# Optimization experiments

Measured on AMD Instinct MI355X. Metric: run time of the kernel, lower is better.

## Reference

```python
import jax, jax.numpy as jnp
import numpy as np

B, N, C = 16, 65536, 21          # batch, anchors, classes (class 0 = background)
TH_CONF = 0.05                   # confidence threshold
TH_IOU = 0.5                     # NMS IoU threshold
TOP_K = 200                      # candidates kept per (batch, class) before NMS
V0, V1 = 0.1, 0.2                # SSD box-coder variances


def setup_inputs() -> dict:
    key = jax.random.key(0)
    k1, k2, k3, k4 = jax.random.split(key, 4)
    conf = jax.random.normal(k1, (B, N, C), dtype=jnp.float32)
    loc = jax.random.normal(k2, (B, N, 4), dtype=jnp.float32)
    # anchors in center form (cx, cy, w, h), normalized coords
    cxcy = jax.random.uniform(k3, (N, 2), dtype=jnp.float32)
    wh = 0.02 + 0.2 * jax.random.uniform(k4, (N, 2), dtype=jnp.float32)
    anchors = jnp.concatenate([cxcy, wh], axis=-1)
    return {"conf": conf, "loc": loc, "anchors": anchors}


def _decode(anchors, loc):
    # SSD decode: anchors [N,4] center form, loc [B,N,4] offsets -> [B,N,4] xyxy
    a_xy, a_wh = anchors[:, :2], anchors[:, 2:]
    xy = a_xy + loc[..., :2] * V0 * a_wh
    wh = a_wh * jnp.exp(loc[..., 2:] * V1)
    return jnp.concatenate([xy - 0.5 * wh, xy + 0.5 * wh], axis=-1)


def _iou(boxes):
    # boxes [K,4] xyxy -> pairwise IoU [K,K]
    area = jnp.maximum(boxes[:, 2] - boxes[:, 0], 0.0) * jnp.maximum(boxes[:, 3] - boxes[:, 1], 0.0)
    lt = jnp.maximum(boxes[:, None, :2], boxes[None, :, :2])
    rb = jnp.minimum(boxes[:, None, 2:], boxes[None, :, 2:])
    wh = jnp.maximum(rb - lt, 0.0)
    inter = wh[..., 0] * wh[..., 1]
    union = area[:, None] + area[None, :] - inter
    return inter / jnp.maximum(union, 1e-9)


def _nms_keep(iou, valid):
    # greedy NMS over score-sorted candidates; valid = (score >= TH_CONF)
    K = iou.shape[0]
    idx = jnp.arange(K)

    def body(keep, xs):
        row, v, i = xs
        suppressed = jnp.any((row > TH_IOU) & keep & (idx < i))
        k = v & (~suppressed)
        return keep.at[i].set(k), 0

    keep, _ = jax.lax.scan(body, jnp.zeros((K,), dtype=bool), (iou, valid, idx))
    return keep


def reference(conf, loc, anchors):
    score = jax.nn.softmax(conf, axis=2)            # [B,N,C]
    boxes = _decode(anchors, loc)                   # [B,N,4]
    # skip background class 0 (cls_base = 1 for softmax classifier)
    cls_scores = jnp.swapaxes(score[..., 1:], 1, 2)  # [B,C-1,N]
    top_s, top_i = jax.lax.top_k(cls_scores, TOP_K)  # [B,C-1,K], sorted desc
    top_boxes = jax.vmap(lambda bx, ix: bx[ix])(boxes, top_i)  # [B,C-1,K,4]
    valid = top_s >= TH_CONF
    keep = jax.vmap(jax.vmap(lambda b, v: _nms_keep(_iou(b), v)))(top_boxes, valid)  # [B,C-1,K]
    out_boxes = jnp.where(keep[..., None], top_boxes, 0.0)
    out_scores = jnp.where(keep, top_s, 0.0)
    return jnp.concatenate([out_boxes, out_scores[..., None]], axis=-1)  # [B,C-1,K,5]
```

## Files before the change

### kernel.cpp

```cpp
#include <hip/hip_runtime.h>
#include <stdint.h>

#define NB     16
#define NANCH  65536
#define NC     21
#define NCLS   20
#define NCOL   (NB * NCLS)
#define TOPK   200
#define NBINS  1024
#define CAP    256
#define CAPCOL 4096
#define CAPLDS 2048
#define CNTSTRIDE 16

constexpr float TH      = 0.05f;
constexpr float TPRE    = 0.20f;
constexpr float SCALE20 = (float)NBINS / 0.80f;
constexpr float SCALE05 = (float)NBINS / 0.95f;

__device__ __forceinline__ int bin20(float s) {
  int b = (int)((s - 0.20f) * SCALE20);
  return b < 0 ? 0 : (b > NBINS - 1 ? NBINS - 1 : b);
}
__device__ __forceinline__ int bin05(float s) {
  int b = (int)((s - 0.05f) * SCALE05);
  return b < 0 ? 0 : (b > NBINS - 1 ? NBINS - 1 : b);
}

__device__ __forceinline__ unsigned long long shflx64(unsigned long long v, int m) {
  unsigned int lo = (unsigned int)v, hi = (unsigned int)(v >> 32);
  lo = __shfl_xor(lo, m);
  hi = __shfl_xor(hi, m);
  return ((unsigned long long)hi << 32) | lo;
}
__device__ __forceinline__ unsigned long long rl64(unsigned long long v, int lane) {
  unsigned int lo = __builtin_amdgcn_readlane((int)(unsigned int)v, lane);
  unsigned int hi = __builtin_amdgcn_readlane((int)(unsigned int)(v >> 32), lane);
  return ((unsigned long long)hi << 32) | lo;
}

__device__ __forceinline__ void softmax_tail(const float* x, float* e, float& S) {
  float m = x[0];
#pragma unroll
  for (int c = 1; c < NC; ++c) m = fmaxf(m, x[c]);
#pragma unroll
  for (int c = 0; c < NC; ++c) e[c] = expf(x[c] - m);
  float r0 = e[0] + e[8],  r1 = e[1] + e[9],  r2 = e[2] + e[10], r3 = e[3] + e[11];
  float r4 = e[4] + e[12], r5 = e[5] + e[13], r6 = e[6] + e[14], r7 = e[7] + e[15];
  S = ((r0 + r1) + (r2 + r3)) + ((r4 + r5) + (r6 + r7));
  S += e[16]; S += e[17]; S += e[18]; S += e[19]; S += e[20];
}

__global__ __launch_bounds__(256) void softmax_collect_kernel(
    const float* __restrict__ conf,
    unsigned int* __restrict__ cnt, unsigned long long* __restrict__ cand) {
  const int tid = threadIdx.x;
  __shared__ float ld[256 * NC];
  const float4* src = (const float4*)conf + (long long)blockIdx.x * 1344;
  float4* dst4 = (float4*)ld;
#pragma unroll
  for (int i = 0; i < 5; ++i) dst4[tid + i * 256] = src[tid + i * 256];
  if (tid < 64) dst4[tid + 1280] = src[tid + 1280];
  __syncthreads();

  const int a = blockIdx.x * 256 + tid;
  const int b = a >> 16;
  const int n = a & (NANCH - 1);
  float x[NC];
#pragma unroll
  for (int c = 0; c < NC; ++c) x[c] = ld[tid * NC + c];
  float e[NC], S;
  softmax_tail(x, e, S);
  const float t = TPRE * S;
  unsigned int takemask = 0;
#pragma unroll
  for (int c = 0; c < NCLS; ++c)
    if (e[c + 1] >= t) takemask |= (1u << c);

  __shared__ unsigned int wcnt[4][NCLS];
  __shared__ unsigned int wbase[4][NCLS];
  const int wave = tid >> 6, lane = tid & 63;
#pragma unroll
  for (int c = 0; c < NCLS; ++c) {
    unsigned long long m = __ballot((takemask >> c) & 1);
    if (lane == 0) wcnt[wave][c] = (unsigned int)__popcll(m);
  }
  __syncthreads();
  if (tid < NCLS) {
    const int c = tid;
    unsigned int t0 = wcnt[0][c], t1 = wcnt[1][c], t2 = wcnt[2][c], t3 = wcnt[3][c];
    unsigned int tot = t0 + t1 + t2 + t3;
    unsigned int base = tot ? atomicAdd(&cnt[(b * NCLS + c) * CNTSTRIDE], tot) : 0u;
    wbase[0][c] = base;
    wbase[1][c] = base + t0;
    wbase[2][c] = base + t0 + t1;
    wbase[3][c] = base + t0 + t1 + t2;
  }
  __syncthreads();
#pragma unroll
  for (int c = 0; c < NCLS; ++c) {
    bool take = (takemask >> c) & 1;
    unsigned long long m = __ballot(take);
    if (take) {
      float s = e[c + 1] / S;
      unsigned int off = wbase[wave][c] +
                         (unsigned int)__popcll(m & ((1ULL << lane) - 1));
      if (off < CAPCOL) {
        unsigned int key = __float_as_uint(s) | 0x80000000u;
        cand[(long long)(b * NCLS + c) * CAPCOL + off] =
            ((unsigned long long)(key ^ 0xFFFFFFFFu) << 32) |
            (unsigned long long)(unsigned int)n;
      }
    }
  }
}

__device__ __forceinline__ int find_sel(unsigned int* hist, unsigned int* part,
                                        int* s_sel, int tid) {
  unsigned int p = hist[tid*4] + hist[tid*4+1] + hist[tid*4+2] + hist[tid*4+3];
  part[tid] = p;
  if (tid == 0) *s_sel = -1;
  __syncthreads();
  if (tid < 64) {
    unsigned int p4 = part[tid*4] + part[tid*4+1] + part[tid*4+2] + part[tid*4+3];
    unsigned int sfx = p4;
#pragma unroll
    for (int off = 1; off < 64; off <<= 1) {
      unsigned int o = __shfl_down(sfx, off);
      if (tid + off < 64) sfx += o;
    }
    unsigned int above = sfx - p4;
    if (above < TOPK && sfx >= TOPK) {
      unsigned int cum = above; int sel = tid * 16; bool found = false;
      for (int q = 3; q >= 0 && !found; --q) {
        unsigned int pc = part[tid*4 + q];
        if (cum + pc >= TOPK) {
          for (int i = 3; i >= 0; --i) {
            unsigned int c = hist[(tid*4+q)*4 + i];
            if (cum + c >= TOPK) { sel = (tid*4+q)*4 + i; found = true; break; }
            cum += c;
          }
        } else cum += pc;
      }
      *s_sel = sel;
    }
  }
  __syncthreads();
  return *s_sel;
}

__global__ __launch_bounds__(256) void topk_nms_kernel(
    const unsigned long long* __restrict__ candg,
    const unsigned int* __restrict__ cnt,
    const float* __restrict__ conf, const float* __restrict__ loc,
    const float* __restrict__ anchors, float* __restrict__ out) {
  const int bc = blockIdx.x;
  const int b  = bc / NCLS;
  const int cls = bc % NCLS;
  const int tid = threadIdx.x;

  __shared__ unsigned long long cg_lds[CAPLDS];
  __shared__ unsigned int hist[NBINS];
  __shared__ unsigned int part[256];
  __shared__ int s_sel, s_n;
  __shared__ unsigned long long cand[CAP];
  __shared__ float4 box4[TOPK];
  __shared__ float sscore[TOPK];
  __shared__ unsigned long long adj[TOPK][4];
  __shared__ unsigned long long keptw[4];

  int nc = (int)cnt[bc * CNTSTRIDE];
  const bool fast = (nc >= TOPK && nc <= CAPLDS);
  for (int i = tid; i < NBINS; i += 256) hist[i] = 0;
  if (tid == 0) s_n = 0;

  const unsigned long long* cg = candg + (long long)bc * CAPCOL;
  if (fast) {
    const int npair = nc >> 1;
    const ulonglong2* cg2 = (const ulonglong2*)cg;
    for (int i = tid; i < npair; i += 256) {
      ulonglong2 v2 = cg2[i];
      cg_lds[2 * i]     = v2.x;
      cg_lds[2 * i + 1] = v2.y;
    }
    if ((nc & 1) && tid == 0) cg_lds[nc - 1] = cg[nc - 1];
    __syncthreads();
    for (int i = tid; i < nc; i += 256) {
      unsigned int key = (unsigned int)(cg_lds[i] >> 32) ^ 0xFFFFFFFFu;
      float s = __uint_as_float(key ^ 0x80000000u);
      atomicAdd(&hist[bin20(s)], 1u);
    }
    __syncthreads();
    int sel = find_sel(hist, part, &s_sel, tid);
    for (int i = tid; i < nc; i += 256) {
      unsigned long long k64 = cg_lds[i];
      unsigned int key = (unsigned int)(k64 >> 32) ^ 0xFFFFFFFFu;
      float s = __uint_as_float(key ^ 0x80000000u);
      if (bin20(s) >= sel) {
        int pos = atomicAdd(&s_n, 1);
        if (pos < CAP) cand[pos] = k64;
      }
    }
  } else {
    __syncthreads();
    for (int n = tid; n < NANCH; n += 256) {
      const float* row = conf + ((long long)b * NANCH + n) * NC;
      float x[NC], e[NC], S;
#pragma unroll
      for (int c = 0; c < NC; ++c) x[c] = row[c];
      softmax_tail(x, e, S);
      float s = e[cls + 1] / S;
      if (s >= TH) atomicAdd(&hist[bin05(s)], 1u);
    }
    __syncthreads();
    int sel = find_sel(hist, part, &s_sel, tid);
    for (int n = tid; n < NANCH; n += 256) {
      const float* row = conf + ((long long)b * NANCH + n) * NC;
      float x[NC], e[NC], S;
#pragma unroll
      for (int c = 0; c < NC; ++c) x[c] = row[c];
      softmax_tail(x, e, S);
      float s = e[cls + 1] / S;
      if (s >= TH && (sel < 0 || bin05(s) >= sel)) {
        int pos = atomicAdd(&s_n, 1);
        if (pos < CAP) {
          unsigned int key = __float_as_uint(s) | 0x80000000u;
          cand[pos] = ((unsigned long long)(key ^ 0xFFFFFFFFu) << 32) |
                      (unsigned long long)(unsigned int)n;
        }
      }
    }
  }
  __syncthreads();
  int ncand = s_n; if (ncand > CAP) ncand = CAP;

  unsigned long long v = (tid < ncand) ? cand[tid] : ~0ULL;
  for (int k = 2; k <= CAP; k <<= 1) {
    const bool up = ((tid & k) == 0);
    for (int j = k >> 1; j >= 64; j >>= 1) {
      cand[tid] = v;
      __syncthreads();
      unsigned long long o = cand[tid ^ j];
      bool keepMin = (((tid & j) == 0) == up);
      v = ((v < o) == keepMin) ? v : o;
      __syncthreads();
    }
    for (int j = (k >> 1) < 32 ? (k >> 1) : 32; j >= 1; j >>= 1) {
      unsigned long long o = shflx64(v, j);
      bool keepMin = (((tid & j) == 0) == up);
      v = ((v < o) == keepMin) ? v : o;
    }
  }
  const int nsel = (ncand < TOPK) ? ncand : TOPK;

  if (tid < TOPK) {
    if (tid < nsel) {
      unsigned int key = (unsigned int)(v >> 32) ^ 0xFFFFFFFFu;
      float s = __uint_as_float(key ^ 0x80000000u);
      int idx = (int)(unsigned int)(v & 0xFFFFFFFFu);
      float4 anc = ((const float4*)anchors)[idx];
      float4 l   = ((const float4*)loc)[(long long)b * NANCH + idx];
      float cx = anc.x + (l.x * 0.1f) * anc.z;
      float cy = anc.y + (l.y * 0.1f) * anc.w;
      float w  = anc.z * expf(l.z * 0.2f);
      float h  = anc.w * expf(l.w * 0.2f);
      box4[tid] = make_float4(cx - 0.5f * w, cy - 0.5f * h,
                              cx + 0.5f * w, cy + 0.5f * h);
      sscore[tid] = s;
    } else {
      box4[tid] = make_float4(0.f, 0.f, 0.f, 0.f);
      sscore[tid] = 0.0f;
    }
  }
  __syncthreads();

  if (tid < TOPK) {
    const float4 a4 = box4[tid];
    const float aar = fmaxf(a4.z - a4.x, 0.f) * fmaxf(a4.w - a4.y, 0.f);
    const int myw = tid >> 6, myb = tid & 63;
#pragma unroll 1
    for (int w = 0; w < 4; ++w) {
      const int jend = (w < 3) ? 64 : (TOPK - 192);
      unsigned long long roww = 0;
#pragma unroll 4
      for (int jj = 0; jj < jend; ++jj) {
        const int j = (w << 6) + jj;
        float4 b4 = box4[j];
        float jar = fmaxf(b4.z - b4.x, 0.f) * fmaxf(b4.w - b4.y, 0.f);
        float ltx = fmaxf(a4.x, b4.x);
        float lty = fmaxf(a4.y, b4.y);
        float rbx = fminf(a4.z, b4.z);
        float rby = fminf(a4.w, b4.w);
        float iw = fmaxf(rbx - ltx, 0.0f);
        float ih = fmaxf(rby - lty, 0.0f);
        float inter = iw * ih;
        float uni = aar + jar - inter;
        float um = fmaxf(uni, 1e-9f);
        float half = 0.5f * um;
        bool hit;
        if (inter > half * 1.000001f)      hit = true;
        else if (inter < half * 0.999999f) hit = false;
        else                               hit = (inter / um > 0.5f);
        roww |= (unsigned long long)(hit ? 1u : 0u) << jj;
      }
      unsigned long long tri = (w < myw) ? 0ULL
                             : (w > myw) ? ~0ULL
                             : ((myb == 63) ? 0ULL : (~0ULL << (myb + 1)));
      adj[tid][w] = roww & tri;
    }
  }
  __syncthreads();

  if (tid < 64) {
    const int l = tid;
    unsigned long long r0[4], r1[4], r2[4], r3[4];
#pragma unroll
    for (int w = 0; w < 4; ++w) {
      r0[w] = adj[l][w];
      r1[w] = adj[l + 64][w];
      r2[w] = adj[l + 128][w];
      r3[w] = (l < 8) ? adj[l + 192][w] : 0ULL;
    }
    unsigned long long sup0 = 0, sup1 = 0, sup2 = 0, sup3 = 0;
    unsigned long long k0 = 0, k1 = 0, k2 = 0, k3 = 0;
#pragma unroll 1
    for (int ii = 0; ii < 64; ++ii) {
      unsigned long long live = ((~sup0 >> ii) & 1ULL) &
                                (unsigned long long)(ii < nsel);
      unsigned long long mask = 0ULL - live;
      k0 |= live << ii;
      sup0 |= rl64(r0[0], ii) & mask; sup1 |= rl64(r0[1], ii) & mask;
      sup2 |= rl64(r0[2], ii) & mask; sup3 |= rl64(r0[3], ii) & mask;
    }
#pragma unroll 1
    for (int ii = 0; ii < 64; ++ii) {
      unsigned long long live = ((~sup1 >> ii) & 1ULL) &
                                (unsigned long long)((64 + ii) < nsel);
      unsigned long long mask = 0ULL - live;
      k1 |= live << ii;
      sup1 |= rl64(r1[1], ii) & mask; sup2 |= rl64(r1[2], ii) & mask;
      sup3 |= rl64(r1[3], ii) & mask;
    }
#pragma unroll 1
    for (int ii = 0; ii < 64; ++ii) {
      unsigned long long live = ((~sup2 >> ii) & 1ULL) &
                                (unsigned long long)((128 + ii) < nsel);
      unsigned long long mask = 0ULL - live;
      k2 |= live << ii;
      sup2 |= rl64(r2[2], ii) & mask; sup3 |= rl64(r2[3], ii) & mask;
    }
#pragma unroll 1
    for (int ii = 0; ii < 8; ++ii) {
      unsigned long long live = ((~sup3 >> ii) & 1ULL) &
                                (unsigned long long)((192 + ii) < nsel);
      unsigned long long mask = 0ULL - live;
      k3 |= live << ii;
      sup3 |= rl64(r3[3], ii) & mask;
    }
    if (l == 0) { keptw[0] = k0; keptw[1] = k1; keptw[2] = k2; keptw[3] = k3; }
  }
  __syncthreads();

  const float* fb = (const float*)box4;
  float* ob = out + (long long)bc * (TOPK * 5);
  for (int pos = tid; pos < TOPK * 5; pos += 256) {
    int row = pos / 5;
    int k5  = pos - row * 5;
    bool kp = (keptw[row >> 6] >> (row & 63)) & 1ULL;
    float val = (k5 == 4) ? sscore[row] : fb[row * 4 + k5];
    ob[pos] = kp ? val : 0.0f;
  }
}

extern "C" void kernel_launch(void* const* d_in, const int* in_sizes, int n_in,
                              void* d_out, int out_size, void* d_ws, size_t ws_size,
                              hipStream_t stream) {
  const float* conf    = (const float*)d_in[0];
  const float* loc     = (const float*)d_in[1];
  const float* anchors = (const float*)d_in[2];
  float* out = (float*)d_out;

  char* ws = (char*)d_ws;
  unsigned long long* cand = (unsigned long long*)ws;
  unsigned int*       cnt  = (unsigned int*)(ws + 10485760);

  hipMemsetAsync(ws + 10485760, 0, 320 * CNTSTRIDE * 4, stream);
  softmax_collect_kernel<<<(NB * NANCH) / 256, 256, 0, stream>>>(conf, cnt, cand);
  topk_nms_kernel<<<NCOL, 256, 0, stream>>>(cand, cnt, conf, loc, anchors, out);
}
```

Baseline: 100.4 us.

## Widen top-k/NMS blocks to 1024 threads and split IoU rows by word

Launches the per-(batch,class) top-k/NMS kernel with 1024 threads instead of 256 and inlines the histogram selection helper. The IoU adjacency build now gives each thread one 64-bit word of a row instead of looping over four, so it uses 800 threads. Loads, histogramming and output writes stride by 1024, while the bitonic sort is gated to the first 256 threads. The goal is to shorten the serial per-block latency of the 320 blocks, at the cost of more barriers across 16 waves and lower occupancy per CU.

```diff
diff --git a/kernel.cpp b/kernel.cpp
--- a/kernel.cpp
+++ b/kernel.cpp
@@ -115,11 +115,67 @@
   }
 }
 
-__device__ __forceinline__ int find_sel(unsigned int* hist, unsigned int* part,
-                                        int* s_sel, int tid) {
-  unsigned int p = hist[tid*4] + hist[tid*4+1] + hist[tid*4+2] + hist[tid*4+3];
-  part[tid] = p;
-  if (tid == 0) *s_sel = -1;
+__global__ __launch_bounds__(1024) void topk_nms_kernel(
+    const unsigned long long* __restrict__ candg,
+    const unsigned int* __restrict__ cnt,
+    const float* __restrict__ conf, const float* __restrict__ loc,
+    const float* __restrict__ anchors, float* __restrict__ out) {
+  const int bc = blockIdx.x;
+  const int b  = bc / NCLS;
+  const int cls = bc % NCLS;
+  const int tid = threadIdx.x;
+
+  __shared__ unsigned long long cg_lds[CAPLDS];
+  __shared__ unsigned int hist[NBINS];
+  __shared__ unsigned int part[256];
+  __shared__ int s_sel, s_n;
+  __shared__ unsigned long long cand[CAP];
+  __shared__ float4 box4[TOPK];
+  __shared__ float sscore[TOPK];
+  __shared__ unsigned long long adj[TOPK][4];
+  __shared__ unsigned long long keptw[4];
+
+  int nc = (int)cnt[bc * CNTSTRIDE];
+  const bool fast = (nc >= TOPK && nc <= CAPLDS);
+  for (int i = tid; i < NBINS; i += 1024) hist[i] = 0;
+  if (tid == 0) s_n = 0;
+  __syncthreads();
+
+  const unsigned long long* cg = candg + (long long)bc * CAPCOL;
+  if (fast) {
+    const int npair = nc >> 1;
+    const ulonglong2* cg2 = (const ulonglong2*)cg;
+    for (int i = tid; i < npair; i += 1024) {
+      ulonglong2 v2 = cg2[i];
+      cg_lds[2 * i]     = v2.x;
+      cg_lds[2 * i + 1] = v2.y;
+    }
+    if ((nc & 1) && tid == 0) cg_lds[nc - 1] = cg[nc - 1];
+  }
+  __syncthreads();
+
+  if (fast) {
+    for (int i = tid; i < nc; i += 1024) {
+      unsigned int key = (unsigned int)(cg_lds[i] >> 32) ^ 0xFFFFFFFFu;
+      float s = __uint_as_float(key ^ 0x80000000u);
+      atomicAdd(&hist[bin20(s)], 1u);
+    }
+  } else {
+    for (int n = tid; n < NANCH; n += 1024) {
+      const float* row = conf + ((long long)b * NANCH + n) * NC;
+      float x[NC], e[NC], S;
+#pragma unroll
+      for (int c = 0; c < NC; ++c) x[c] = row[c];
+      softmax_tail(x, e, S);
+      float s = e[cls + 1] / S;
+      if (s >= TH) atomicAdd(&hist[bin05(s)], 1u);
+    }
+  }
+  __syncthreads();
+
+  if (tid < 256)
+    part[tid] = hist[tid*4] + hist[tid*4+1] + hist[tid*4+2] + hist[tid*4+3];
+  if (tid == 0) s_sel = -1;
   __syncthreads();
   if (tid < 64) {
     unsigned int p4 = part[tid*4] + part[tid*4+1] + part[tid*4+2] + part[tid*4+3];
@@ -142,57 +198,14 @@
           }
         } else cum += pc;
       }
-      *s_sel = sel;
-    }
-  }
-  __syncthreads();
-  return *s_sel;
-}
-
-__global__ __launch_bounds__(256) void topk_nms_kernel(
-    const unsigned long long* __restrict__ candg,
-    const unsigned int* __restrict__ cnt,
-    const float* __restrict__ conf, const float* __restrict__ loc,
-    const float* __restrict__ anchors, float* __restrict__ out) {
-  const int bc = blockIdx.x;
-  const int b  = bc / NCLS;
-  const int cls = bc % NCLS;
-  const int tid = threadIdx.x;
-
-  __shared__ unsigned long long cg_lds[CAPLDS];
-  __shared__ unsigned int hist[NBINS];
-  __shared__ unsigned int part[256];
-  __shared__ int s_sel, s_n;
-  __shared__ unsigned long long cand[CAP];
-  __shared__ float4 box4[TOPK];
-  __shared__ float sscore[TOPK];
-  __shared__ unsigned long long adj[TOPK][4];
-  __shared__ unsigned long long keptw[4];
-
-  int nc = (int)cnt[bc * CNTSTRIDE];
-  const bool fast = (nc >= TOPK && nc <= CAPLDS);
-  for (int i = tid; i < NBINS; i += 256) hist[i] = 0;
-  if (tid == 0) s_n = 0;
-
-  const unsigned long long* cg = candg + (long long)bc * CAPCOL;
+      s_sel = sel;
+    }
+  }
+  __syncthreads();
+  const int sel = s_sel;
+
   if (fast) {
-    const int npair = nc >> 1;
-    const ulonglong2* cg2 = (const ulonglong2*)cg;
-    for (int i = tid; i < npair; i += 256) {
-      ulonglong2 v2 = cg2[i];
-      cg_lds[2 * i]     = v2.x;
-      cg_lds[2 * i + 1] = v2.y;
-    }
-    if ((nc & 1) && tid == 0) cg_lds[nc - 1] = cg[nc - 1];
-    __syncthreads();
-    for (int i = tid; i < nc; i += 256) {
-      unsigned int key = (unsigned int)(cg_lds[i] >> 32) ^ 0xFFFFFFFFu;
-      float s = __uint_as_float(key ^ 0x80000000u);
-      atomicAdd(&hist[bin20(s)], 1u);
-    }
-    __syncthreads();
-    int sel = find_sel(hist, part, &s_sel, tid);
-    for (int i = tid; i < nc; i += 256) {
+    for (int i = tid; i < nc; i += 1024) {
       unsigned long long k64 = cg_lds[i];
       unsigned int key = (unsigned int)(k64 >> 32) ^ 0xFFFFFFFFu;
       float s = __uint_as_float(key ^ 0x80000000u);
@@ -202,19 +215,7 @@
       }
     }
   } else {
-    __syncthreads();
-    for (int n = tid; n < NANCH; n += 256) {
-      const float* row = conf + ((long long)b * NANCH + n) * NC;
-      float x[NC], e[NC], S;
-#pragma unroll
-      for (int c = 0; c < NC; ++c) x[c] = row[c];
-      softmax_tail(x, e, S);
-      float s = e[cls + 1] / S;
-      if (s >= TH) atomicAdd(&hist[bin05(s)], 1u);
-    }
-    __syncthreads();
-    int sel = find_sel(hist, part, &s_sel, tid);
-    for (int n = tid; n < NANCH; n += 256) {
+    for (int n = tid; n < NANCH; n += 1024) {
       const float* row = conf + ((long long)b * NANCH + n) * NC;
       float x[NC], e[NC], S;
 #pragma unroll
@@ -238,17 +239,21 @@
   for (int k = 2; k <= CAP; k <<= 1) {
     const bool up = ((tid & k) == 0);
     for (int j = k >> 1; j >= 64; j >>= 1) {
-      cand[tid] = v;
+      if (tid < 256) cand[tid] = v;
       __syncthreads();
-      unsigned long long o = cand[tid ^ j];
-      bool keepMin = (((tid & j) == 0) == up);
-      v = ((v < o) == keepMin) ? v : o;
+      if (tid < 256) {
+        unsigned long long o = cand[tid ^ j];
+        bool keepMin = (((tid & j) == 0) == up);
+        v = ((v < o) == keepMin) ? v : o;
+      }
       __syncthreads();
     }
-    for (int j = (k >> 1) < 32 ? (k >> 1) : 32; j >= 1; j >>= 1) {
-      unsigned long long o = shflx64(v, j);
-      bool keepMin = (((tid & j) == 0) == up);
-      v = ((v < o) == keepMin) ? v : o;
+    if (tid < 256) {
+      for (int j = (k >> 1) < 32 ? (k >> 1) : 32; j >= 1; j >>= 1) {
+        unsigned long long o = shflx64(v, j);
+        bool keepMin = (((tid & j) == 0) == up);
+        v = ((v < o) == keepMin) ? v : o;
+      }
     }
   }
   const int nsel = (ncand < TOPK) ? ncand : TOPK;
@@ -274,40 +279,38 @@
   }
   __syncthreads();
 
-  if (tid < TOPK) {
-    const float4 a4 = box4[tid];
+  if (tid < TOPK * 4) {
+    const int row = tid >> 2, w = tid & 3;
+    const float4 a4 = box4[row];
     const float aar = fmaxf(a4.z - a4.x, 0.f) * fmaxf(a4.w - a4.y, 0.f);
-    const int myw = tid >> 6, myb = tid & 63;
-#pragma unroll 1
-    for (int w = 0; w < 4; ++w) {
-      const int jend = (w < 3) ? 64 : (TOPK - 192);
-      unsigned long long roww = 0;
+    const int jend = (w < 3) ? 64 : (TOPK - 192);
+    unsigned long long roww = 0;
 #pragma unroll 4
-      for (int jj = 0; jj < jend; ++jj) {
-        const int j = (w << 6) + jj;
-        float4 b4 = box4[j];
-        float jar = fmaxf(b4.z - b4.x, 0.f) * fmaxf(b4.w - b4.y, 0.f);
-        float ltx = fmaxf(a4.x, b4.x);
-        float lty = fmaxf(a4.y, b4.y);
-        float rbx = fminf(a4.z, b4.z);
-        float rby = fminf(a4.w, b4.w);
-        float iw = fmaxf(rbx - ltx, 0.0f);
-        float ih = fmaxf(rby - lty, 0.0f);
-        float inter = iw * ih;
-        float uni = aar + jar - inter;
-        float um = fmaxf(uni, 1e-9f);
-        float half = 0.5f * um;
-        bool hit;
-        if (inter > half * 1.000001f)      hit = true;
-        else if (inter < half * 0.999999f) hit = false;
-        else                               hit = (inter / um > 0.5f);
-        roww |= (unsigned long long)(hit ? 1u : 0u) << jj;
-      }
-      unsigned long long tri = (w < myw) ? 0ULL
-                             : (w > myw) ? ~0ULL
-                             : ((myb == 63) ? 0ULL : (~0ULL << (myb + 1)));
-      adj[tid][w] = roww & tri;
-    }
+    for (int jj = 0; jj < jend; ++jj) {
+      const int j = (w << 6) + jj;
+      float4 b4 = box4[j];
+      float jar = fmaxf(b4.z - b4.x, 0.f) * fmaxf(b4.w - b4.y, 0.f);
+      float ltx = fmaxf(a4.x, b4.x);
+      float lty = fmaxf(a4.y, b4.y);
+      float rbx = fminf(a4.z, b4.z);
+      float rby = fminf(a4.w, b4.w);
+      float iw = fmaxf(rbx - ltx, 0.0f);
+      float ih = fmaxf(rby - lty, 0.0f);
+      float inter = iw * ih;
+      float uni = aar + jar - inter;
+      float um = fmaxf(uni, 1e-9f);
+      float half = 0.5f * um;
+      bool hit;
+      if (inter > half * 1.000001f)      hit = true;
+      else if (inter < half * 0.999999f) hit = false;
+      else                               hit = (inter / um > 0.5f);
+      roww |= (unsigned long long)(hit ? 1u : 0u) << jj;
+    }
+    const int myw = row >> 6, myb = row & 63;
+    unsigned long long tri = (w < myw) ? 0ULL
+                           : (w > myw) ? ~0ULL
+                           : ((myb == 63) ? 0ULL : (~0ULL << (myb + 1)));
+    adj[row][w] = roww & tri;
   }
   __syncthreads();
 
@@ -363,7 +366,7 @@
 
   const float* fb = (const float*)box4;
   float* ob = out + (long long)bc * (TOPK * 5);
-  for (int pos = tid; pos < TOPK * 5; pos += 256) {
+  for (int pos = tid; pos < TOPK * 5; pos += 1024) {
     int row = pos / 5;
     int k5  = pos - row * 5;
     bool kp = (keptw[row >> 6] >> (row & 63)) & 1ULL;
@@ -386,5 +389,5 @@
 
   hipMemsetAsync(ws + 10485760, 0, 320 * CNTSTRIDE * 4, stream);
   softmax_collect_kernel<<<(NB * NANCH) / 256, 256, 0, stream>>>(conf, cnt, cand);
-  topk_nms_kernel<<<NCOL, 256, 0, stream>>>(cand, cnt, conf, loc, anchors, out);
-}
+  topk_nms_kernel<<<NCOL, 1024, 0, stream>>>(cand, cnt, conf, loc, anchors, out);
+}
```

After: 92.09 us (median of 2 runs). -8.3%, faster.
